# Kernel optimization log

Measured on AMD Instinct MI355X. Metric: run time of the kernel, lower is better.

Reference implementation:

```python
import jax, jax.numpy as jnp
import numpy as np

N_NODES = 50000
N_EDGES = 600000
N_HID = 128
N_HEAD = 8
EPS = 1e-5


def _degrees(src, dst, n):
    ones = jnp.ones(src.shape[0], dtype=jnp.float32)
    indeg = jax.ops.segment_sum(ones, dst, num_segments=n)
    outdeg = jax.ops.segment_sum(ones, src, num_segments=n)
    return indeg, outdeg


def _sage_gcn(x, src, dst, indeg, W, b):
    # DGL SAGEConv(aggregator_type='gcn'), eval mode (feat_drop identity):
    # h = fc_neigh((sum_neigh + self) / (in_deg + 1)) + bias
    agg = jax.ops.segment_sum(x[src], dst, num_segments=x.shape[0])
    hn = (agg + x) / (indeg[:, None] + 1.0)
    return hn @ W + b


def _graph_conv(x, src, dst, indeg, outdeg, W, b):
    # DGL GraphConv(norm='both', allow_zero_in_degree=True):
    # out = D_in^{-1/2} A D_out^{-1/2} X W + b  (inf norms -> 0)
    norm_s = jnp.where(outdeg > 0, jax.lax.rsqrt(jnp.maximum(outdeg, 1.0)), 0.0)
    norm_d = jnp.where(indeg > 0, jax.lax.rsqrt(jnp.maximum(indeg, 1.0)), 0.0)
    feat = (x @ W) * norm_s[:, None]  # weight first (in_feats > out_feats)
    agg = jax.ops.segment_sum(feat[src], dst, num_segments=x.shape[0])
    return agg * norm_d[:, None] + b


def _layer_norm(x, g, b):
    mu = jnp.mean(x, axis=-1, keepdims=True)
    var = jnp.mean(jnp.square(x - mu), axis=-1, keepdims=True)
    return (x - mu) * jax.lax.rsqrt(var + EPS) * g + b


def _forward(h, gt_src, gt_dst, attr_src, attr_dst,
             W1, b1, W2, b2, W3, b3, ffn_W1, ffn_b1, ffn_W2, ffn_b2, ln_g, ln_b):
    n = h.shape[0]
    gt_in, gt_out = _degrees(gt_src, gt_dst, n)
    at_in, at_out = _degrees(attr_src, attr_dst, n)
    # branch -> graph pattern for n_head == 8: gt, gt, attr, attr, gt, gt, attr, attr
    graphs = [(gt_src, gt_dst, gt_in, gt_out), (gt_src, gt_dst, gt_in, gt_out),
              (attr_src, attr_dst, at_in, at_out), (attr_src, attr_dst, at_in, at_out)] * 2
    x0 = h.reshape(-1, N_HID)
    outs = []
    for i in range(N_HEAD):
        src, dst, indeg, outdeg = graphs[i]
        o = _sage_gcn(x0, src, dst, indeg, W1[i], b1[i])
        o = _sage_gcn(o, src, dst, indeg, W2[i], b2[i])
        o = _graph_conv(o, src, dst, indeg, outdeg, W3[i], b3[i])
        outs.append(o)
    x = jnp.concatenate(outs, axis=-1).reshape(h.shape)
    x = h + _layer_norm(x, ln_g, ln_b)
    ffn = jax.nn.relu(x @ ffn_W1 + ffn_b1) @ ffn_W2 + ffn_b2
    return x + _layer_norm(ffn, ln_g, ln_b)


def setup_inputs() -> dict:
    key = jax.random.key(0)
    ks = jax.random.split(key, 12)
    s = 1.0 / np.sqrt(N_HID)
    return {
        "h": jax.random.normal(ks[0], (N_NODES, N_HID), dtype=jnp.float32),
        "gt_src": jax.random.randint(ks[1], (N_EDGES,), 0, N_NODES, dtype=jnp.int32),
        "gt_dst": jax.random.randint(ks[2], (N_EDGES,), 0, N_NODES, dtype=jnp.int32),
        "attr_src": jax.random.randint(ks[3], (N_EDGES,), 0, N_NODES, dtype=jnp.int32),
        "attr_dst": jax.random.randint(ks[4], (N_EDGES,), 0, N_NODES, dtype=jnp.int32),
        "W1": jax.random.normal(ks[5], (N_HEAD, N_HID, N_HID), dtype=jnp.float32) * s,
        "b1": jnp.zeros((N_HEAD, N_HID), dtype=jnp.float32),
        "W2": jax.random.normal(ks[6], (N_HEAD, N_HID, N_HID), dtype=jnp.float32) * s,
        "b2": jnp.zeros((N_HEAD, N_HID), dtype=jnp.float32),
        "W3": jax.random.normal(ks[7], (N_HEAD, N_HID, N_HID // N_HEAD), dtype=jnp.float32) * s,
        "b3": jnp.zeros((N_HEAD, N_HID // N_HEAD), dtype=jnp.float32),
        "ffn_W1": jax.random.normal(ks[8], (N_HID, N_HID), dtype=jnp.float32) * s,
        "ffn_b1": jnp.zeros((N_HID,), dtype=jnp.float32),
        "ffn_W2": jax.random.normal(ks[9], (N_HID, N_HID), dtype=jnp.float32) * s,
        "ffn_b2": jnp.zeros((N_HID,), dtype=jnp.float32),
        "ln_g": jnp.ones((N_HID,), dtype=jnp.float32),
        "ln_b": jnp.zeros((N_HID,), dtype=jnp.float32),
    }


def reference(h, gt_src, gt_dst, attr_src, attr_dst,
              W1, b1, W2, b2, W3, b3, ffn_W1, ffn_b1, ffn_W2, ffn_b2, ln_g, ln_b):
    return _forward(h, gt_src, gt_dst, attr_src, attr_dst,
                    W1, b1, W2, b2, W3, b3, ffn_W1, ffn_b1, ffn_W2, ffn_b2, ln_g, ln_b)
```

## Files before the change

kernel.cpp:

```cpp
#include <hip/hip_runtime.h>

#define DD 128
#define NHEAD 8
#define DH 16
#define EPS 1e-5f
#define BSH 9
#define BWIDTH 512
#define NBLK1 256

typedef __attribute__((ext_vector_type(8))) short bf16x8;
typedef __attribute__((ext_vector_type(4))) float f32x4;

__device__ inline unsigned short f2b(float f) {
    unsigned u = __float_as_uint(f);
    u += 0x7fffu + ((u >> 16) & 1);
    return (unsigned short)(u >> 16);
}
__device__ inline unsigned pk2(float lo, float hi) {
    return (unsigned)f2b(lo) | ((unsigned)f2b(hi) << 16);
}
__device__ inline void upacc(uint4 u, float* a) {
    a[0] += __uint_as_float(u.x << 16);
    a[1] += __uint_as_float(u.x & 0xffff0000u);
    a[2] += __uint_as_float(u.y << 16);
    a[3] += __uint_as_float(u.y & 0xffff0000u);
    a[4] += __uint_as_float(u.z << 16);
    a[5] += __uint_as_float(u.z & 0xffff0000u);
    a[6] += __uint_as_float(u.w << 16);
    a[7] += __uint_as_float(u.w & 0xffff0000u);
}

#define SWZB(row, off) ((off) ^ (((row) & 7) << 4))

__global__ void k_h2b(const float4* __restrict__ h4, ushort4* __restrict__ hb, int n4) {
    int i = blockIdx.x * 256 + threadIdx.x;
    if (i < n4) {
        float4 v = h4[i];
        hb[i] = make_ushort4(f2b(v.x), f2b(v.y), f2b(v.z), f2b(v.w));
    }
}

__global__ __launch_bounds__(256) void k_p1count(
        const int* __restrict__ gs, const int* __restrict__ gd,
        const int* __restrict__ as_, const int* __restrict__ ad,
        int* __restrict__ blkcnt, int E, int N, int Btot) {
    __shared__ int cnts[512];
    for (int j = threadIdx.x; j < 2 * Btot; j += 256) cnts[j] = 0;
    __syncthreads();
    int E2 = 2 * E;
    for (int i = blockIdx.x * 256 + threadIdx.x; i < E2; i += NBLK1 * 256) {
        int g = (i >= E);
        int e = g ? i - E : i;
        int s = g ? as_[e] : gs[e];
        int d = g ? ad[e] : gd[e];
        int cd = d + g * N, cs = s + g * N;
        atomicAdd(&cnts[cd >> BSH], 1);
        atomicAdd(&cnts[Btot + (cs >> BSH)], 1);
    }
    __syncthreads();
    for (int j = threadIdx.x; j < 2 * Btot; j += 256)
        blkcnt[j * NBLK1 + blockIdx.x] = cnts[j];
}

__global__ void k_scan1(const int* __restrict__ cnt, int* __restrict__ outv,
                        int* __restrict__ part, int n) {
    __shared__ int wsums[4];
    int t = threadIdx.x;
    int base = blockIdx.x * 1024 + t * 4;
    int v0 = 0, v1 = 0, v2 = 0, v3 = 0;
    if (base + 3 < n) {
        int4 q = *(const int4*)(cnt + base);
        v0 = q.x; v1 = q.y; v2 = q.z; v3 = q.w;
    } else {
        if (base < n)     v0 = cnt[base];
        if (base + 1 < n) v1 = cnt[base + 1];
        if (base + 2 < n) v2 = cnt[base + 2];
        if (base + 3 < n) v3 = cnt[base + 3];
    }
    int s0 = v0, s1 = s0 + v1, s2 = s1 + v2, s3 = s2 + v3;
    int x = s3;
    int lane = t & 63, w = t >> 6;
    for (int o = 1; o < 64; o <<= 1) { int u = __shfl_up(x, o); if (lane >= o) x += u; }
    if (lane == 63) wsums[w] = x;
    __syncthreads();
    int wo = 0;
    for (int i = 0; i < w; ++i) wo += wsums[i];
    int excl = wo + x - s3;
    if (base < n)     outv[base]     = excl;
    if (base + 1 < n) outv[base + 1] = excl + s0;
    if (base + 2 < n) outv[base + 2] = excl + s1;
    if (base + 3 < n) outv[base + 3] = excl + s2;
    if (t == 255) part[blockIdx.x] = wo + x;
}

__global__ void k_scan2(int* __restrict__ part, int nb) {
    __shared__ int ws[4];
    int t = threadIdx.x;
    int v = (t < nb) ? part[t] : 0;
    int x = v;
    int lane = t & 63, w = t >> 6;
    for (int o = 1; o < 64; o <<= 1) { int u = __shfl_up(x, o); if (lane >= o) x += u; }
    if (lane == 63) ws[w] = x;
    __syncthreads();
    int wo = 0;
    for (int i = 0; i < w; ++i) wo += ws[i];
    if (t < nb) part[t] = wo + x - v;
}

__global__ void k_scan3(int* __restrict__ outv, const int* __restrict__ part, int n, int total) {
    int i = blockIdx.x * blockDim.x + threadIdx.x;
    if (i < n) outv[i] += part[i >> 10];
    if (i == 0) outv[n] = total;
}

__global__ __launch_bounds__(256) void k_p1scatter(
        const int* __restrict__ gs, const int* __restrict__ gd,
        const int* __restrict__ as_, const int* __restrict__ ad,
        const int* __restrict__ scn, unsigned* __restrict__ pairs,
        unsigned short* __restrict__ svals, int E, int N, int Btot) {
    __shared__ int cur[512];
    for (int j = threadIdx.x; j < 2 * Btot; j += 256)
        cur[j] = scn[j * NBLK1 + blockIdx.x];
    __syncthreads();
    int E2 = 2 * E;
    for (int i = blockIdx.x * 256 + threadIdx.x; i < E2; i += NBLK1 * 256) {
        int g = (i >= E);
        int e = g ? i - E : i;
        int s = g ? as_[e] : gs[e];
        int d = g ? ad[e] : gd[e];
        int cd = d + g * N, cs = s + g * N;
        int pd = atomicAdd(&cur[cd >> BSH], 1);
        pairs[pd] = ((unsigned)(cd & (BWIDTH - 1)) << 16) | (unsigned)s;
        int ps = atomicAdd(&cur[Btot + (cs >> BSH)], 1);
        svals[ps - E2] = (unsigned short)(cs & (BWIDTH - 1));
    }
}

__global__ __launch_bounds__(256) void k_p2(
        const unsigned* __restrict__ pairs, const unsigned short* __restrict__ svals,
        const int* __restrict__ scn, int* __restrict__ rowptr, int* __restrict__ csr,
        float* __restrict__ indeg, float* __restrict__ norms,
        int E, int N2, int Btot) {
    __shared__ int hist[BWIDTH];
    __shared__ int offs[BWIDTH];
    __shared__ int cur[BWIDTH];
    __shared__ int ws4[4];
    int b = blockIdx.x, t = threadIdx.x;
    int node0 = b << BSH;
    int W = N2 - node0; if (W > BWIDTH) W = BWIDTH;
    int Sd = scn[b * NBLK1], Ed = scn[(b + 1) * NBLK1];
    hist[t] = 0; hist[t + 256] = 0;
    __syncthreads();
    for (int i = Sd + t; i < Ed; i += 256)
        atomicAdd(&hist[pairs[i] >> 16], 1);
    __syncthreads();
    int a0 = hist[2 * t], a1 = hist[2 * t + 1];
    int sum2 = a0 + a1;
    int lane = t & 63, w = t >> 6;
    int x = sum2;
    for (int o = 1; o < 64; o <<= 1) { int u = __shfl_up(x, o); if (lane >= o) x += u; }
    if (lane == 63) ws4[w] = x;
    __syncthreads();
    int wo = 0;
    for (int i = 0; i < w; ++i) wo += ws4[i];
    int excl2 = wo + x - sum2;
    offs[2 * t] = excl2; offs[2 * t + 1] = excl2 + a0;
    cur[t] = 0; cur[t + 256] = 0;
    __syncthreads();
    for (int j = t; j < W; j += 256) {
        rowptr[node0 + j] = Sd + offs[j];
        indeg[node0 + j] = (float)hist[j];
    }
    if (b == 0 && t == 0) rowptr[N2] = 2 * E;
    for (int i = Sd + t; i < Ed; i += 256) {
        unsigned p = pairs[i];
        int l = p >> 16;
        int pos = atomicAdd(&cur[l], 1);
        csr[Sd + offs[l] + pos] = (int)(p & 0xffffu);
    }
    __syncthreads();
    hist[t] = 0; hist[t + 256] = 0;
    __syncthreads();
    int Ss = scn[(Btot + b) * NBLK1] - 2 * E;
    int Es = scn[(Btot + b + 1) * NBLK1] - 2 * E;
    for (int i = Ss + t; i < Es; i += 256)
        atomicAdd(&hist[svals[i]], 1);
    __syncthreads();
    for (int j = t; j < W; j += 256) {
        int od = hist[j];
        norms[node0 + j] = od > 0 ? rsqrtf((float)od) : 0.f;
    }
}

__global__ __launch_bounds__(256) void k_pull_avgF(
        const uint4* __restrict__ xb, const int* __restrict__ rowptr,
        const int* __restrict__ csr, const float* __restrict__ norms,
        uint4* __restrict__ outb, float* __restrict__ ssum,
        int N, int shared_in, int doscale) {
    int cd = blockIdx.x * 16 + (threadIdx.x >> 4);
    int lane = threadIdx.x & 15;
    if (cd >= 2 * N) return;
    int gofs = (cd >= N) ? N : 0;
    int base = shared_in ? 0 : gofs;
    int beg = rowptr[cd], end = rowptr[cd + 1];
    float a[8];
    {
        uint4 u = xb[(size_t)(base + cd - gofs) * 16 + lane];
        a[0] = __uint_as_float(u.x << 16); a[1] = __uint_as_float(u.x & 0xffff0000u);
        a[2] = __uint_as_float(u.y << 16); a[3] = __uint_as_float(u.y & 0xffff0000u);
        a[4] = __uint_as_float(u.z << 16); a[5] = __uint_as_float(u.z & 0xffff0000u);
        a[6] = __uint_as_float(u.w << 16); a[7] = __uint_as_float(u.w & 0xffff0000u);
    }
    float ss = 0.f;
    int e = beg;
    int nb = end - e; if (nb > 16) nb = 16;
    int idx = (lane < nb) ? csr[e + lane] : 0;
    while (nb > 0) {
        int en = e + nb;
        int nbn = end - en; if (nbn > 16) nbn = 16;
        int idxn = (lane < nbn) ? csr[en + lane] : 0;
        #pragma unroll 8
        for (int d = 0; d < nb; ++d) {
            int s = __shfl(idx, d, 16);
            upacc(xb[(size_t)(base + s) * 16 + lane], a);
            if (doscale) ss += norms[base + s];
        }
        e = en; nb = nbn; idx = idxn;
    }
    float sc = 1.f / (float)(end - beg + 1);
    if (doscale) sc *= norms[cd];
    uint4 o;
    o.x = pk2(a[0] * sc, a[1] * sc); o.y = pk2(a[2] * sc, a[3] * sc);
    o.z = pk2(a[4] * sc, a[5] * sc); o.w = pk2(a[6] * sc, a[7] * sc);
    outb[(size_t)cd * 16 + lane] = o;
    if (doscale && lane == 0) ssum[cd] = ss;
}

__global__ __launch_bounds__(256) void k_pull_sumF(
        const uint4* __restrict__ Pb, const int* __restrict__ rowptr,
        const int* __restrict__ csr, uint4* __restrict__ Qb, int N) {
    int cd = blockIdx.x * 16 + (threadIdx.x >> 4);
    int lane = threadIdx.x & 15;
    if (cd >= 2 * N) return;
    int base = (cd >= N) ? N : 0;
    int beg = rowptr[cd], end = rowptr[cd + 1];
    float a[8] = {0.f, 0.f, 0.f, 0.f, 0.f, 0.f, 0.f, 0.f};
    int e = beg;
    int nb = end - e; if (nb > 16) nb = 16;
    int idx = (lane < nb) ? csr[e + lane] : 0;
    while (nb > 0) {
        int en = e + nb;
        int nbn = end - en; if (nbn > 16) nbn = 16;
        int idxn = (lane < nbn) ? csr[en + lane] : 0;
        #pragma unroll 8
        for (int d = 0; d < nb; ++d) {
            int s = __shfl(idx, d, 16);
            upacc(Pb[(size_t)(base + s) * 16 + lane], a);
        }
        e = en; nb = nbn; idx = idxn;
    }
    uint4 o;
    o.x = pk2(a[0], a[1]); o.y = pk2(a[2], a[3]);
    o.z = pk2(a[4], a[5]); o.w = pk2(a[6], a[7]);
    Qb[(size_t)cd * 16 + lane] = o;
}

__global__ __launch_bounds__(256) void k_wT(
        const float* __restrict__ W2, const float* __restrict__ W3, float* __restrict__ T) {
    int t = threadIdx.x;
    int o = blockIdx.x * 16 + (t >> 4);
    int sub = t & 15;
    int i = o >> 11, oo = o & 2047;
    int r = oo >> 4, c = oo & 15;
    const float* w2 = W2 + (size_t)i * DD * DD + r * DD + sub * 8;
    const float* w3 = W3 + (size_t)i * DD * DH + c + sub * 8 * DH;
    float acc = 0.f;
    #pragma unroll
    for (int k = 0; k < 8; ++k) acc += w2[k] * w3[k * DH];
    #pragma unroll
    for (int m = 8; m; m >>= 1) acc += __shfl_xor(acc, m);
    if (sub == 0) T[o] = acc;
}

__global__ __launch_bounds__(256) void k_wM(
        const float* __restrict__ W1, const float* __restrict__ T,
        unsigned short* __restrict__ Mtb) {
    int t = threadIdx.x;
    int o = blockIdx.x * 16 + (t >> 4);
    int sub = t & 15;
    int i = o >> 11, oo = o & 2047;
    int r = oo >> 4, c = oo & 15;
    const float* w1 = W1 + (size_t)i * DD * DD + r * DD + sub * 8;
    const float* tt = T + (size_t)i * DD * DH + c + sub * 8 * DH;
    float acc = 0.f;
    #pragma unroll
    for (int k = 0; k < 8; ++k) acc += w1[k] * tt[k * DH];
    #pragma unroll
    for (int m = 8; m; m >>= 1) acc += __shfl_xor(acc, m);
    if (sub == 0) Mtb[(size_t)(i * DH + c) * DD + r] = f2b(acc);
}

__global__ __launch_bounds__(256) void k_cvec2(
        const float* __restrict__ b1, const float* __restrict__ b2,
        const float* __restrict__ T, const float* __restrict__ W3,
        float* __restrict__ cvec) {
    int i = blockIdx.x, t = threadIdx.x;
    int c = t >> 4, sub = t & 15;
    const float* tt = T + (size_t)i * DD * DH + c + sub * 8 * DH;
    const float* w3 = W3 + (size_t)i * DD * DH + c + sub * 8 * DH;
    const float* p1 = b1 + i * DD + sub * 8;
    const float* p2 = b2 + i * DD + sub * 8;
    float acc = 0.f;
    #pragma unroll
    for (int k = 0; k < 8; ++k) acc += p1[k] * tt[k * DH] + p2[k] * w3[k * DH];
    #pragma unroll
    for (int m = 8; m; m >>= 1) acc += __shfl_xor(acc, m);
    if (sub == 0) cvec[i * DH + c] = acc;
}

__global__ void k_wtb2(const float* __restrict__ fW1, const float* __restrict__ fW2,
                       unsigned short* __restrict__ W1tb, unsigned short* __restrict__ W2tb) {
    int idx = blockIdx.x * 256 + threadIdx.x;
    int which = idx >> 14;
    int o = idx & 16383;
    int c = o >> 7, k = o & 127;
    const float* W = which ? fW2 : fW1;
    unsigned short* Wt = which ? W2tb : W1tb;
    Wt[c * DD + k] = f2b(W[(size_t)k * DD + c]);
}

__global__ __launch_bounds__(256) void k_tailm(
        const unsigned short* __restrict__ Qgtb, const unsigned short* __restrict__ Qatb,
        const float* __restrict__ ssum, const float* __restrict__ indeg,
        const unsigned short* __restrict__ Mtb, const unsigned short* __restrict__ W1tb,
        const unsigned short* __restrict__ W2tb,
        const float* __restrict__ cvec, const float* __restrict__ b3,
        const float* __restrict__ h, const float* __restrict__ ln_g,
        const float* __restrict__ ln_b, const float* __restrict__ Fb1,
        const float* __restrict__ Fb2, float* __restrict__ out, int N) {
    __shared__ __align__(16) unsigned short A0[64 * DD];
    __shared__ __align__(16) unsigned short A1[64 * DD];
    __shared__ __align__(16) unsigned short Bt[DD * DD];
    int t = threadIdx.x;
    int w = t >> 6, l = t & 63;
    int lm = l & 15, lk = l >> 4;
    int row0 = blockIdx.x * 64;

    for (int i = t; i < 1024; i += 256) {
        int r = i >> 4, ch = i & 15;
        int gr = row0 + r; if (gr >= N) gr = N - 1;
        uint4 v0 = *(const uint4*)(Qgtb + (size_t)gr * DD + ch * 8);
        uint4 v1 = *(const uint4*)(Qatb + (size_t)gr * DD + ch * 8);
        *(uint4*)((char*)A0 + r * 256 + SWZB(r, ch * 16)) = v0;
        *(uint4*)((char*)A1 + r * 256 + SWZB(r, ch * 16)) = v1;
    }
    for (int i = t; i < 2048; i += 256) {
        int c = i >> 4, ch = i & 15;
        uint4 v = *(const uint4*)(Mtb + (size_t)c * DD + ch * 8);
        *(uint4*)((char*)Bt + c * 256 + SWZB(c, ch * 16)) = v;
    }
    __syncthreads();

    int arow = w * 16 + lm;
    int abase = arow * 256;

    f32x4 acc[8];
    #pragma unroll
    for (int i = 0; i < 8; ++i) acc[i] = (f32x4){0.f, 0.f, 0.f, 0.f};
    #pragma unroll
    for (int kt = 0; kt < 4; ++kt) {
        int aoff = abase + SWZB(arow, kt * 64 + lk * 16);
        bf16x8 ag = *(const bf16x8*)((const char*)A0 + aoff);
        bf16x8 aa = *(const bf16x8*)((const char*)A1 + aoff);
        #pragma unroll
        for (int ct = 0; ct < 8; ++ct) {
            int bc = ct * 16 + lm;
            bf16x8 b = *(const bf16x8*)((const char*)Bt + bc * 256 + SWZB(bc, kt * 64 + lk * 16));
            acc[ct] = __builtin_amdgcn_mfma_f32_16x16x32_bf16(
                ((ct >> 1) & 1) ? aa : ag, b, acc[ct], 0, 0, 0);
        }
    }

    int rbase = row0 + w * 16 + lk * 4;
    float ssv[2][4], ndv[2][4];
    #pragma unroll
    for (int i = 0; i < 4; ++i) {
        int rc = rbase + i; if (rc >= N) rc = N - 1;
        #pragma unroll
        for (int g2 = 0; g2 < 2; ++g2) {
            ssv[g2][i] = ssum[g2 * N + rc];
            float id = indeg[g2 * N + rc];
            ndv[g2][i] = id > 0.f ? rsqrtf(id) : 0.f;
        }
    }
    float glr[8], blr[8];
    #pragma unroll
    for (int ct = 0; ct < 8; ++ct) {
        glr[ct] = ln_g[ct * 16 + lm];
        blr[ct] = ln_b[ct * 16 + lm];
    }
    float vv[8][4];
    float s[4] = {0, 0, 0, 0}, s2[4] = {0, 0, 0, 0};
    #pragma unroll
    for (int ct = 0; ct < 8; ++ct) {
        int col = ct * 16 + lm;
        int g2 = (ct >> 1) & 1;
        float cvv = cvec[col], b3v = b3[col];
        #pragma unroll
        for (int i = 0; i < 4; ++i) {
            float v = (acc[ct][i] + ssv[g2][i] * cvv) * ndv[g2][i] + b3v;
            vv[ct][i] = v;
            s[i] += v; s2[i] += v * v;
        }
    }
    #pragma unroll
    for (int o = 8; o > 0; o >>= 1) {
        #pragma unroll
        for (int i = 0; i < 4; ++i) {
            s[i] += __shfl_xor(s[i], o);
            s2[i] += __shfl_xor(s2[i], o);
        }
    }
    __syncthreads();
    float xk[8][4];
    #pragma unroll
    for (int i = 0; i < 4; ++i) {
        float mu = s[i] * (1.f / DD);
        float var = s2[i] * (1.f / DD) - mu * mu;
        float rs = rsqrtf(var + EPS);
        int row = rbase + i; int rc = row < N ? row : N - 1;
        int lrow = w * 16 + lk * 4 + i;
        #pragma unroll
        for (int ct = 0; ct < 8; ++ct) {
            int col = ct * 16 + lm;
            float x = h[(size_t)rc * DD + col] + (vv[ct][i] - mu) * rs * glr[ct] + blr[ct];
            xk[ct][i] = x;
            *(unsigned short*)((char*)A0 + lrow * 256 + SWZB(lrow, 2 * col)) = f2b(x);
        }
    }
    for (int i = t; i < 2048; i += 256) {
        int c = i >> 4, ch = i & 15;
        uint4 v = *(const uint4*)(W1tb + (size_t)c * DD + ch * 8);
        *(uint4*)((char*)Bt + c * 256 + SWZB(c, ch * 16)) = v;
    }
    __syncthreads();

    f32x4 ac2[8];
    #pragma unroll
    for (int i = 0; i < 8; ++i) ac2[i] = (f32x4){0.f, 0.f, 0.f, 0.f};
    #pragma unroll
    for (int kt = 0; kt < 4; ++kt) {
        bf16x8 a = *(const bf16x8*)((const char*)A0 + abase + SWZB(arow, kt * 64 + lk * 16));
        #pragma unroll
        for (int ct = 0; ct < 8; ++ct) {
            int bc = ct * 16 + lm;
            bf16x8 b = *(const bf16x8*)((const char*)Bt + bc * 256 + SWZB(bc, kt * 64 + lk * 16));
            ac2[ct] = __builtin_amdgcn_mfma_f32_16x16x32_bf16(a, b, ac2[ct], 0, 0, 0);
        }
    }
    #pragma unroll
    for (int i = 0; i < 4; ++i) {
        int lrow = w * 16 + lk * 4 + i;
        #pragma unroll
        for (int ct = 0; ct < 8; ++ct) {
            int col = ct * 16 + lm;
            float f = ac2[ct][i] + Fb1[col];
            *(unsigned short*)((char*)A1 + lrow * 256 + SWZB(lrow, 2 * col)) =
                f2b(f > 0.f ? f : 0.f);
        }
    }
    __syncthreads();
    for (int i = t; i < 2048; i += 256) {
        int c = i >> 4, ch = i & 15;
        uint4 v = *(const uint4*)(W2tb + (size_t)c * DD + ch * 8);
        *(uint4*)((char*)Bt + c * 256 + SWZB(c, ch * 16)) = v;
    }
    __syncthreads();

    f32x4 ac3[8];
    #pragma unroll
    for (int i = 0; i < 8; ++i) ac3[i] = (f32x4){0.f, 0.f, 0.f, 0.f};
    #pragma unroll
    for (int kt = 0; kt < 4; ++kt) {
        bf16x8 a = *(const bf16x8*)((const char*)A1 + abase + SWZB(arow, kt * 64 + lk * 16));
        #pragma unroll
        for (int ct = 0; ct < 8; ++ct) {
            int bc = ct * 16 + lm;
            bf16x8 b = *(const bf16x8*)((const char*)Bt + bc * 256 + SWZB(bc, kt * 64 + lk * 16));
            ac3[ct] = __builtin_amdgcn_mfma_f32_16x16x32_bf16(a, b, ac3[ct], 0, 0, 0);
        }
    }
    float v3[8][4];
    float s3[4] = {0, 0, 0, 0}, s32[4] = {0, 0, 0, 0};
    #pragma unroll
    for (int ct = 0; ct < 8; ++ct) {
        float fb = Fb2[ct * 16 + lm];
        #pragma unroll
        for (int i = 0; i < 4; ++i) {
            float v = ac3[ct][i] + fb;
            v3[ct][i] = v;
            s3[i] += v; s32[i] += v * v;
        }
    }
    #pragma unroll
    for (int o = 8; o > 0; o >>= 1) {
        #pragma unroll
        for (int i = 0; i < 4; ++i) {
            s3[i] += __shfl_xor(s3[i], o);
            s32[i] += __shfl_xor(s32[i], o);
        }
    }
    #pragma unroll
    for (int i = 0; i < 4; ++i) {
        float mu = s3[i] * (1.f / DD);
        float var = s32[i] * (1.f / DD) - mu * mu;
        float rs = rsqrtf(var + EPS);
        int row = rbase + i;
        if (row < N) {
            #pragma unroll
            for (int ct = 0; ct < 8; ++ct) {
                int col = ct * 16 + lm;
                out[(size_t)row * DD + col] = xk[ct][i] + (v3[ct][i] - mu) * rs * glr[ct] + blr[ct];
            }
        }
    }
}

extern "C" void kernel_launch(void* const* d_in, const int* in_sizes, int n_in,
                              void* d_out, int out_size, void* d_ws, size_t ws_size,
                              hipStream_t stream) {
    const float* h      = (const float*)d_in[0];
    const int*   gt_src = (const int*)d_in[1];
    const int*   gt_dst = (const int*)d_in[2];
    const int*   at_src = (const int*)d_in[3];
    const int*   at_dst = (const int*)d_in[4];
    const float* W1     = (const float*)d_in[5];
    const float* b1     = (const float*)d_in[6];
    const float* W2     = (const float*)d_in[7];
    const float* b2     = (const float*)d_in[8];
    const float* W3     = (const float*)d_in[9];
    const float* b3     = (const float*)d_in[10];
    const float* fW1    = (const float*)d_in[11];
    const float* fb1    = (const float*)d_in[12];
    const float* fW2    = (const float*)d_in[13];
    const float* fb2    = (const float*)d_in[14];
    const float* ln_g   = (const float*)d_in[15];
    const float* ln_b   = (const float*)d_in[16];

    const int E = in_sizes[1];
    const int N = in_sizes[0] / DD;
    const size_t NB = (size_t)N * DD;
    const int N2 = 2 * N;
    const int Btot = (N2 + BWIDTH - 1) >> BSH;
    const int n1 = 2 * Btot * NBLK1;

    unsigned short* hb   = (unsigned short*)d_ws;
    unsigned short* bufA = hb + NB;
    unsigned short* bufB = bufA + 2 * NB;
    float* sm = (float*)(bufB + 2 * NB);
    float* norms = sm;  sm += N2;
    float* indeg = sm;  sm += N2;
    float* ssum  = sm;  sm += N2;
    float* cvec  = sm;  sm += NHEAD * DH + 32;
    float* Tm    = sm;  sm += NHEAD * DD * DH;
    unsigned short* Mtb  = (unsigned short*)sm;
    unsigned short* W1tb = Mtb + DD * DD;
    unsigned short* W2tb = W1tb + DD * DD;
    int* ip = (int*)(W2tb + DD * DD);
    int* rowptr = ip;  ip += ((N2 + 1 + 3) & ~3);
    int* csr    = ip;  ip += 2 * E;
    int* blkcnt = ip;  ip += ((n1 + 1 + 3) & ~3);
    int* scn    = ip;  ip += ((n1 + 1 + 3) & ~3);
    int* part   = ip;  ip += 256;
    unsigned* pairs = (unsigned*)bufA;
    unsigned short* svals = (unsigned short*)(pairs + 2 * E);

    k_wT   <<<1024, 256, 0, stream>>>(W2, W3, Tm);
    k_wM   <<<1024, 256, 0, stream>>>(W1, Tm, Mtb);
    k_cvec2<<<NHEAD, 256, 0, stream>>>(b1, b2, Tm, W3, cvec);
    k_wtb2 <<<128, 256, 0, stream>>>(fW1, fW2, W1tb, W2tb);

    const int TB = 256;
    k_h2b<<<(int)(NB / 4 + TB - 1) / TB, TB, 0, stream>>>((const float4*)h, (ushort4*)hb,
                                                          (int)(NB / 4));
    k_p1count<<<NBLK1, 256, 0, stream>>>(gt_src, gt_dst, at_src, at_dst, blkcnt, E, N, Btot);
    int nsb = (n1 + 1023) / 1024;
    k_scan1<<<nsb, 256, 0, stream>>>(blkcnt, scn, part, n1);
    k_scan2<<<1, 256, 0, stream>>>(part, nsb);
    k_scan3<<<(n1 + TB - 1) / TB, TB, 0, stream>>>(scn, part, n1, 4 * E);
    k_p1scatter<<<NBLK1, 256, 0, stream>>>(gt_src, gt_dst, at_src, at_dst, scn,
                                           pairs, svals, E, N, Btot);
    k_p2<<<Btot, 256, 0, stream>>>(pairs, svals, scn, rowptr, csr, indeg, norms,
                                   E, N2, Btot);

    const int pgrid2 = (N2 + 15) / 16;
    k_pull_avgF<<<pgrid2, 256, 0, stream>>>((const uint4*)hb, rowptr, csr, norms,
                                            (uint4*)bufB, ssum, N, 1, 0);
    k_pull_avgF<<<pgrid2, 256, 0, stream>>>((const uint4*)bufB, rowptr, csr, norms,
                                            (uint4*)bufA, ssum, N, 0, 1);
    k_pull_sumF<<<pgrid2, 256, 0, stream>>>((const uint4*)bufA, rowptr, csr,
                                            (uint4*)bufB, N);
    unsigned short* Qb = bufB;

    k_tailm<<<(N + 63) / 64, 256, 0, stream>>>(Qb, Qb + NB, ssum, indeg, Mtb, W1tb, W2tb,
                                               cvec, b3, h, ln_g, ln_b, fb1, fb2,
                                               (float*)d_out, N);
}
```

Baseline: 245.6 us.

## Fuse final neighbor-sum gather into the tail MFMA kernel via shared memory

Measured after the change: 304.8 us. 24.1% more time.

```diff
diff --git a/kernel.cpp b/kernel.cpp
--- a/kernel.cpp
+++ b/kernel.cpp
@@ -236,35 +236,6 @@
     if (doscale && lane == 0) ssum[cd] = ss;
 }
 
-__global__ __launch_bounds__(256) void k_pull_sumF(
-        const uint4* __restrict__ Pb, const int* __restrict__ rowptr,
-        const int* __restrict__ csr, uint4* __restrict__ Qb, int N) {
-    int cd = blockIdx.x * 16 + (threadIdx.x >> 4);
-    int lane = threadIdx.x & 15;
-    if (cd >= 2 * N) return;
-    int base = (cd >= N) ? N : 0;
-    int beg = rowptr[cd], end = rowptr[cd + 1];
-    float a[8] = {0.f, 0.f, 0.f, 0.f, 0.f, 0.f, 0.f, 0.f};
-    int e = beg;
-    int nb = end - e; if (nb > 16) nb = 16;
-    int idx = (lane < nb) ? csr[e + lane] : 0;
-    while (nb > 0) {
-        int en = e + nb;
-        int nbn = end - en; if (nbn > 16) nbn = 16;
-        int idxn = (lane < nbn) ? csr[en + lane] : 0;
-        #pragma unroll 8
-        for (int d = 0; d < nb; ++d) {
-            int s = __shfl(idx, d, 16);
-            upacc(Pb[(size_t)(base + s) * 16 + lane], a);
-        }
-        e = en; nb = nbn; idx = idxn;
-    }
-    uint4 o;
-    o.x = pk2(a[0], a[1]); o.y = pk2(a[2], a[3]);
-    o.z = pk2(a[4], a[5]); o.w = pk2(a[6], a[7]);
-    Qb[(size_t)cd * 16 + lane] = o;
-}
-
 __global__ __launch_bounds__(256) void k_wT(
         const float* __restrict__ W2, const float* __restrict__ W3, float* __restrict__ T) {
     int t = threadIdx.x;
@@ -329,8 +300,9 @@
     Wt[c * DD + k] = f2b(W[(size_t)k * DD + c]);
 }
 
-__global__ __launch_bounds__(256) void k_tailm(
-        const unsigned short* __restrict__ Qgtb, const unsigned short* __restrict__ Qatb,
+__global__ __launch_bounds__(256) void k_tailg(
+        const uint4* __restrict__ Pb, const int* __restrict__ rowptr,
+        const int* __restrict__ csr,
         const float* __restrict__ ssum, const float* __restrict__ indeg,
         const unsigned short* __restrict__ Mtb, const unsigned short* __restrict__ W1tb,
         const unsigned short* __restrict__ W2tb,
@@ -346,18 +318,42 @@
     int lm = l & 15, lk = l >> 4;
     int row0 = blockIdx.x * 64;
 
-    for (int i = t; i < 1024; i += 256) {
-        int r = i >> 4, ch = i & 15;
-        int gr = row0 + r; if (gr >= N) gr = N - 1;
-        uint4 v0 = *(const uint4*)(Qgtb + (size_t)gr * DD + ch * 8);
-        uint4 v1 = *(const uint4*)(Qatb + (size_t)gr * DD + ch * 8);
-        *(uint4*)((char*)A0 + r * 256 + SWZB(r, ch * 16)) = v0;
-        *(uint4*)((char*)A1 + r * 256 + SWZB(r, ch * 16)) = v1;
-    }
     for (int i = t; i < 2048; i += 256) {
         int c = i >> 4, ch = i & 15;
         uint4 v = *(const uint4*)(Mtb + (size_t)c * DD + ch * 8);
         *(uint4*)((char*)Bt + c * 256 + SWZB(c, ch * 16)) = v;
+    }
+
+    {
+        int lane = t & 15, task0 = t >> 4;
+        for (int it = 0; it < 8; ++it) {
+            int j = it * 16 + task0;
+            int g = j >> 6, r = j & 63;
+            int row = row0 + r; if (row >= N) row = N - 1;
+            int cd = row + g * N;
+            int base = g * N;
+            int beg = rowptr[cd], end = rowptr[cd + 1];
+            float a[8] = {0.f, 0.f, 0.f, 0.f, 0.f, 0.f, 0.f, 0.f};
+            int e = beg;
+            int nb = end - e; if (nb > 16) nb = 16;
+            int idx = (lane < nb) ? csr[e + lane] : 0;
+            while (nb > 0) {
+                int en = e + nb;
+                int nbn = end - en; if (nbn > 16) nbn = 16;
+                int idxn = (lane < nbn) ? csr[en + lane] : 0;
+                #pragma unroll 8
+                for (int d = 0; d < nb; ++d) {
+                    int s = __shfl(idx, d, 16);
+                    upacc(Pb[(size_t)(base + s) * 16 + lane], a);
+                }
+                e = en; nb = nbn; idx = idxn;
+            }
+            uint4 o;
+            o.x = pk2(a[0], a[1]); o.y = pk2(a[2], a[3]);
+            o.z = pk2(a[4], a[5]); o.w = pk2(a[6], a[7]);
+            unsigned short* P = g ? A1 : A0;
+            *(uint4*)((char*)P + r * 256 + SWZB(r, lane * 16)) = o;
+        }
     }
     __syncthreads();
 
@@ -598,11 +594,9 @@
                                             (uint4*)bufB, ssum, N, 1, 0);
     k_pull_avgF<<<pgrid2, 256, 0, stream>>>((const uint4*)bufB, rowptr, csr, norms,
                                             (uint4*)bufA, ssum, N, 0, 1);
-    k_pull_sumF<<<pgrid2, 256, 0, stream>>>((const uint4*)bufA, rowptr, csr,
-                                            (uint4*)bufB, N);
-    unsigned short* Qb = bufB;
-
-    k_tailm<<<(N + 63) / 64, 256, 0, stream>>>(Qb, Qb + NB, ssum, indeg, Mtb, W1tb, W2tb,
+
+    k_tailg<<<(N + 63) / 64, 256, 0, stream>>>((const uint4*)bufA, rowptr, csr,
+                                               ssum, indeg, Mtb, W1tb, W2tb,
                                                cvec, b3, h, ln_g, ln_b, fb1, fb2,
                                                (float*)d_out, N);
 }
```
